# Kernel optimization log

Measured on AMD Instinct MI355X. Metric: run time of the kernel, lower is better.

## Reference

```python
import jax, jax.numpy as jnp
import numpy as np

N = 49152       # nodes
EH = 8192       # hyperedges (star nodes)
M = N + EH
F = 256         # num_features == expan_dim == MLP_hidden
D = 256
HEADS = 8
CHUNK = 1024
NE_N = 10 * N   # nnz of N x N sparse mats
NE_M = 10 * M   # nnz of M x M sparse mats


def spmm(row, col, val, X, n):
    # sparse [n, m] (COO) @ dense X [m, d] -> [n, d]
    return jax.ops.segment_sum(val[:, None] * X[col], row, num_segments=n)


def expan_net(x, row, col, val, Ws, bs, n):
    # 2-layer GCN: (A @ (X @ W) + b), ReLU between; dropout is identity in eval.
    h = spmm(row, col, val, x @ Ws[0], n) + bs[0]
    h = jax.nn.relu(h)
    return spmm(row, col, val, h @ Ws[1], n) + bs[1]


def chunked_mha(q, k, v, in_w, in_b, out_w, out_b):
    # torch nn.MultiheadAttention on unbatched [L, D] chunks of size CHUNK
    n, d = q.shape
    c = n // CHUNK
    dh = d // HEADS
    wq, wk, wv = jnp.split(in_w, 3, axis=0)
    bq, bk, bv = jnp.split(in_b, 3)
    def resh(t):
        return t.reshape(c, CHUNK, HEADS, dh)
    qh = resh(q @ wq.T + bq)
    kh = resh(k @ wk.T + bk)
    vh = resh(v @ wv.T + bv)
    scale = 1.0 / np.sqrt(dh)
    scores = jnp.einsum('clhe,cmhe->chlm', qh, kh) * scale  # [c,H,CHUNK,CHUNK]
    attn = jax.nn.softmax(scores, axis=-1)
    out = jnp.einsum('chlm,cmhe->clhe', attn, vh).reshape(n, d)
    return out @ out_w.T + out_b


def setup_inputs():
    key = jax.random.key(0)
    ks = iter(jax.random.split(key, 64))
    nrm = lambda shape, s=1.0: jax.random.normal(next(ks), shape, dtype=jnp.float32) * s
    uni = lambda shape: jax.random.uniform(next(ks), shape, dtype=jnp.float32)
    ridx = lambda shape, hi: jax.random.randint(next(ks), shape, 0, hi, dtype=jnp.int32)
    inp = {'x': nrm((N, F))}
    for nm, ne, hi in [('A_cg', NE_N, N), ('A_hyp', NE_N, N), ('A_sg', NE_M, M),
                       ('L_cg', NE_N, N), ('L_hyp', NE_N, N), ('L_sg', NE_M, M)]:
        inp[nm + '_row'] = ridx((ne,), hi)
        inp[nm + '_col'] = ridx((ne,), hi)
        inp[nm + '_val'] = uni((ne,)) * 0.1
    for p in ['cg', 'hg', 'sg']:
        inp[p + '_W'] = nrm((2, F, D), 0.05)
        inp[p + '_b'] = nrm((2, D), 0.05)
    for p in ['sn_hyp', 'sn_cg', 'sn_sg']:
        inp[p + '_W'] = nrm((D, D), 0.05)
        inp[p + '_b'] = nrm((D,), 0.05)
    for p in ['spa', 'spe']:
        for q in ['hyp', 'star', 'clq']:
            inp[f'{p}_{q}_W'] = nrm((D, D), 0.05)
            inp[f'{p}_{q}_b'] = nrm((D,), 0.05)
        inp[p + '_in_w'] = nrm((3 * D, D), 0.05)
        inp[p + '_in_b'] = nrm((3 * D,), 0.05)
        inp[p + '_out_w'] = nrm((D, D), 0.05)
        inp[p + '_out_b'] = nrm((D,), 0.05)
    return inp


def reference(x,
              A_cg_row, A_cg_col, A_cg_val, A_hyp_row, A_hyp_col, A_hyp_val,
              A_sg_row, A_sg_col, A_sg_val, L_cg_row, L_cg_col, L_cg_val,
              L_hyp_row, L_hyp_col, L_hyp_val, L_sg_row, L_sg_col, L_sg_val,
              cg_W, cg_b, hg_W, hg_b, sg_W, sg_b,
              sn_hyp_W, sn_hyp_b, sn_cg_W, sn_cg_b, sn_sg_W, sn_sg_b,
              spa_hyp_W, spa_hyp_b, spa_star_W, spa_star_b, spa_clq_W, spa_clq_b,
              spa_in_w, spa_in_b, spa_out_w, spa_out_b,
              spe_hyp_W, spe_hyp_b, spe_star_W, spe_star_b, spe_clq_W, spe_clq_b,
              spe_in_w, spe_in_b, spe_out_w, spe_out_b):
    n = x.shape[0]
    # star features: nodes first, zero-init hyperedge rows (v_mask == [True]*N+[False]*EH)
    x_star = jnp.concatenate([x, jnp.zeros((EH, x.shape[1]), x.dtype)], axis=0)
    # 1. Expansion graph convolutions
    cg_feat = expan_net(x, A_cg_row, A_cg_col, A_cg_val, cg_W, cg_b, n)
    hg_feat = expan_net(x, A_hyp_row, A_hyp_col, A_hyp_val, hg_W, hg_b, n)
    sg_feat = expan_net(x_star, A_sg_row, A_sg_col, A_sg_val, sg_W, sg_b, n + EH)
    X_star, S_star = sg_feat[:n], sg_feat[n:]
    # 2. SmoothNet: linear then Laplacian spmm
    X_hyp = spmm(L_hyp_row, L_hyp_col, L_hyp_val, hg_feat @ sn_hyp_W.T + sn_hyp_b, n)
    X_cg = spmm(L_cg_row, L_cg_col, L_cg_val, cg_feat @ sn_cg_W.T + sn_cg_b, n)
    X_sg = spmm(L_sg_row, L_sg_col, L_sg_val, sg_feat @ sn_sg_W.T + sn_sg_b, n + EH)
    # 3. TAA attention (chunked MHA, Q/K/V = hyp/star/clique projections)
    X_spectral = chunked_mha(X_hyp @ spe_hyp_W.T + spe_hyp_b,
                             X_cg @ spe_star_W.T + spe_star_b,
                             X_sg[:n] @ spe_clq_W.T + spe_clq_b,
                             spe_in_w, spe_in_b, spe_out_w, spe_out_b)
    X_spatial = chunked_mha(hg_feat @ spa_hyp_W.T + spa_hyp_b,
                            cg_feat @ spa_star_W.T + spa_star_b,
                            X_star @ spa_clq_W.T + spa_clq_b,
                            spa_in_w, spa_in_b, spa_out_w, spa_out_b)
    taa = jnp.concatenate([X_spatial, X_spectral], axis=1)
    return taa, X_star, S_star
```

## Files before the change

kernel.cpp:

```cpp
#include <hip/hip_runtime.h>

#define NN 49152
#define EHN 8192
#define MM (NN + EHN)
#define FD 256
#define DD 256
#define NHEADS 8
#define DHEAD 32
#define CHK 1024
#define NEN (10 * NN)
#define NEM (10 * MM)
#define ROWS_TOT (4 * NN + 2 * MM)
#define ETOT (4 * NEN + 2 * NEM)

typedef __bf16 bf16x8 __attribute__((ext_vector_type(8)));
typedef unsigned short u16x8 __attribute__((ext_vector_type(8)));
typedef float f32x4 __attribute__((ext_vector_type(4)));

static __device__ __forceinline__ unsigned short f2bf(float f) {
  unsigned int u = __float_as_uint(f);
  unsigned int r = (u + 0x7FFFu + ((u >> 16) & 1u)) >> 16;
  return (unsigned short)r;
}
static __device__ __forceinline__ float bf2f(unsigned short u) {
  return __uint_as_float((unsigned int)u << 16);
}
static __device__ __forceinline__ unsigned int cvtpk(float a, float b) {
  unsigned int r;
  asm("v_cvt_pk_bf16_f32 %0, %1, %2" : "=v"(r) : "v"(a), "v"(b));
  return r;
}

struct CastJobs {
  const float* src[8];
  unsigned short* dst[8];
  int trans[8];
};
__global__ __launch_bounds__(256) void cast_w8_kernel(CastJobs jobs)
{
  int job = blockIdx.x >> 8;
  int i = (blockIdx.x & 255) * 256 + threadIdx.x;
  int n = i >> 8, k = i & 255;
  const float* src = jobs.src[job];
  float f = jobs.trans[job] ? src[(size_t)k * 256 + n] : src[i];
  jobs.dst[job][i] = f2bf(f);
}

__global__ __launch_bounds__(256) void combine_w_kernel(
    const float* __restrict__ Bw, const float* __restrict__ Aw,
    const float* __restrict__ ab, const float* __restrict__ bb,
    unsigned short* __restrict__ Wc, float* __restrict__ bc, float fscale)
{
  int n = blockIdx.x, t = threadIdx.x;
  __shared__ float shB[256];
  __shared__ float red[256];
  shB[t] = Bw[n * 256 + t];
  __syncthreads();
  float acc = 0.0f;
  #pragma unroll 8
  for (int j = 0; j < 256; ++j) acc += shB[j] * Aw[j * 256 + t];
  Wc[n * 256 + t] = f2bf(acc * fscale);
  red[t] = shB[t] * ab[t];
  __syncthreads();
  for (int off = 128; off; off >>= 1) {
    if (t < off) red[t] += red[t + off];
    __syncthreads();
  }
  if (t == 0) bc[n] = (red[0] + bb[n]) * fscale;
}

__global__ __launch_bounds__(256) void mm256f_kernel(
    const float* __restrict__ A, const float* __restrict__ B,
    float* __restrict__ C)
{
  int n = blockIdx.x, t = threadIdx.x;
  __shared__ float sa[256];
  sa[t] = A[n * 256 + t];
  __syncthreads();
  float acc = 0.0f;
  #pragma unroll 8
  for (int j = 0; j < 256; ++j) acc += sa[j] * B[j * 256 + t];
  C[n * 256 + t] = acc;
}

__global__ __launch_bounds__(256) void mm256b_kernel(
    const float* __restrict__ A, const float* __restrict__ B,
    unsigned short* __restrict__ W, float fs)
{
  int n = blockIdx.x, t = threadIdx.x;
  __shared__ float sa[256];
  sa[t] = A[n * 256 + t];
  __syncthreads();
  float acc = 0.0f;
  #pragma unroll 8
  for (int j = 0; j < 256; ++j) acc += sa[j] * B[j * 256 + t];
  W[n * 256 + t] = f2bf(acc * fs);
}

__global__ __launch_bounds__(256) void mv256_kernel(
    const float* __restrict__ W, const float* __restrict__ v,
    const float* __restrict__ add, float* __restrict__ outv, float fs)
{
  int t = threadIdx.x;
  __shared__ float sv[256];
  sv[t] = v[t];
  __syncthreads();
  float acc = 0.0f;
  #pragma unroll 8
  for (int k = 0; k < 256; ++k) acc += W[t * 256 + k] * sv[k];
  if (add) acc += add[t];
  outv[t] = fs * acc;
}

struct Gemm3 {
  const void* A[3];
  const unsigned short* W[3];
  const float* c0[3];
  const float* rs[3];
  const float* cvec[3];
  unsigned short* out[3];
  int bs1, bs2, btot;
};
template<int ABF>
__global__ __launch_bounds__(256) void gemm3_kernel(Gemm3 g)
{
  const int b = blockIdx.x;
  const int j = (b >= g.bs2) ? 2 : (b >= g.bs1 ? 1 : 0);
  const int bm = (b - (j == 2 ? g.bs2 : j == 1 ? g.bs1 : 0)) * 64;
  const void* Ain = g.A[j];
  const unsigned short* Wt = g.W[j];

  __shared__ __align__(16) char sA[2][4096];
  __shared__ __align__(16) char sB[2][16384];
  const int tid = threadIdx.x, lane = tid & 63, wid = tid >> 6;
  const int l15 = lane & 15, l4 = lane >> 4;

  f32x4 acc[16] = {};
  const int ar = tid >> 2, akq = (tid & 3) * 8;
  const int bn = tid;

  float4 fa0, fa1;
  u16x8 ua;
  u16x8 rb0, rb1, rb2, rb3;
  auto stage_load = [&](int k0) {
    if (ABF) {
      ua = *(const u16x8*)((const unsigned short*)Ain +
                           (size_t)(bm + ar) * 256 + k0 + akq);
    } else {
      const float* ap = (const float*)Ain + (size_t)(bm + ar) * 256 + k0 + akq;
      fa0 = *(const float4*)ap;
      fa1 = *(const float4*)(ap + 4);
    }
    const unsigned short* bp = Wt + (size_t)bn * 256 + k0;
    rb0 = *(const u16x8*)bp;        rb1 = *(const u16x8*)(bp + 8);
    rb2 = *(const u16x8*)(bp + 16); rb3 = *(const u16x8*)(bp + 24);
  };
  auto stage_write = [&](int buf) {
    u16x8 va;
    if (ABF) {
      va = ua;
    } else {
      va[0] = f2bf(fa0.x); va[1] = f2bf(fa0.y); va[2] = f2bf(fa0.z); va[3] = f2bf(fa0.w);
      va[4] = f2bf(fa1.x); va[5] = f2bf(fa1.y); va[6] = f2bf(fa1.z); va[7] = f2bf(fa1.w);
    }
    int aa = ((ar << 6) + (akq << 1)) ^ ((ar & 7) << 4);
    *(u16x8*)(sA[buf] + aa) = va;
    int bb = (bn << 6) ^ ((bn & 7) << 4);
    *(u16x8*)(sB[buf] + bb) = rb0;
    *(u16x8*)(sB[buf] + (bb ^ 16)) = rb1;
    *(u16x8*)(sB[buf] + (bb ^ 32)) = rb2;
    *(u16x8*)(sB[buf] + (bb ^ 48)) = rb3;
  };

  stage_load(0);
  stage_write(0);
  __syncthreads();
  int cur = 0;
  for (int it = 0; it < 8; ++it) {
    if (it < 7) stage_load((it + 1) * 32);
    int ra = wid * 16 + l15;
    bf16x8 af = *(const bf16x8*)(sA[cur] + ((ra << 6) + (l4 << 4) ^ ((ra & 7) << 4)));
    #pragma unroll
    for (int n4 = 0; n4 < 16; ++n4) {
      int rn = n4 * 16 + l15;
      bf16x8 bf = *(const bf16x8*)(sB[cur] + ((rn << 6) + (l4 << 4) ^ ((rn & 7) << 4)));
      acc[n4] = __builtin_amdgcn_mfma_f32_16x16x32_bf16(af, bf, acc[n4], 0, 0, 0);
    }
    __syncthreads();
    if (it < 7) {
      stage_write(cur ^ 1);
      __syncthreads();
      cur ^= 1;
    }
  }
  const int row = bm + wid * 16 + l4 * 4;
  const float* rs = g.rs[j];
  const float* c0 = g.c0[j];
  const float* cvec = g.cvec[j];
  unsigned short* Cout = g.out[j];
  float rsv[4];
  if (rs) {
    #pragma unroll
    for (int jj = 0; jj < 4; ++jj) rsv[jj] = rs[row + jj];
  }
  #pragma unroll
  for (int n4 = 0; n4 < 16; ++n4) {
    int col = n4 * 16 + l15;
    float base = c0 ? c0[col] : 0.0f;
    float cv = rs ? cvec[col] : 0.0f;
    #pragma unroll
    for (int jj = 0; jj < 4; ++jj) {
      float v = acc[n4][jj] + base;
      if (rs) v += rsv[jj] * cv;
      Cout[(size_t)(row + jj) * 256 + col] = f2bf(v);
    }
  }
}

__global__ __launch_bounds__(256) void gemmout_kernel(
    const unsigned short* __restrict__ Ain, const unsigned short* __restrict__ Wt,
    const float* __restrict__ c0, float* __restrict__ Cout, int coff)
{
  __shared__ __align__(16) char sA[2][4096];
  __shared__ __align__(16) char sB[2][16384];
  const int tid = threadIdx.x, lane = tid & 63, wid = tid >> 6;
  const int l15 = lane & 15, l4 = lane >> 4;
  const int bm = blockIdx.x * 64;

  f32x4 acc[16] = {};
  const int ar = tid >> 2, akq = (tid & 3) * 8;
  const int bn = tid;
  u16x8 ua, rb0, rb1, rb2, rb3;
  auto stage_load = [&](int k0) {
    ua = *(const u16x8*)(Ain + (size_t)(bm + ar) * 256 + k0 + akq);
    const unsigned short* bp = Wt + (size_t)bn * 256 + k0;
    rb0 = *(const u16x8*)bp;        rb1 = *(const u16x8*)(bp + 8);
    rb2 = *(const u16x8*)(bp + 16); rb3 = *(const u16x8*)(bp + 24);
  };
  auto stage_write = [&](int buf) {
    int aa = ((ar << 6) + (akq << 1)) ^ ((ar & 7) << 4);
    *(u16x8*)(sA[buf] + aa) = ua;
    int bb = (bn << 6) ^ ((bn & 7) << 4);
    *(u16x8*)(sB[buf] + bb) = rb0;
    *(u16x8*)(sB[buf] + (bb ^ 16)) = rb1;
    *(u16x8*)(sB[buf] + (bb ^ 32)) = rb2;
    *(u16x8*)(sB[buf] + (bb ^ 48)) = rb3;
  };
  stage_load(0);
  stage_write(0);
  __syncthreads();
  int cur = 0;
  for (int it = 0; it < 8; ++it) {
    if (it < 7) stage_load((it + 1) * 32);
    int ra = wid * 16 + l15;
    bf16x8 af = *(const bf16x8*)(sA[cur] + ((ra << 6) + (l4 << 4) ^ ((ra & 7) << 4)));
    #pragma unroll
    for (int n4 = 0; n4 < 16; ++n4) {
      int rn = n4 * 16 + l15;
      bf16x8 bf = *(const bf16x8*)(sB[cur] + ((rn << 6) + (l4 << 4) ^ ((rn & 7) << 4)));
      acc[n4] = __builtin_amdgcn_mfma_f32_16x16x32_bf16(af, bf, acc[n4], 0, 0, 0);
    }
    __syncthreads();
    if (it < 7) {
      stage_write(cur ^ 1);
      __syncthreads();
      cur ^= 1;
    }
  }
  const int row = bm + wid * 16 + l4 * 4;
  #pragma unroll
  for (int n4 = 0; n4 < 16; ++n4) {
    int col = n4 * 16 + l15;
    float base = c0[col];
    #pragma unroll
    for (int jj = 0; jj < 4; ++jj)
      Cout[(size_t)(row + jj) * 512 + coff + col] = acc[n4][jj] + base;
  }
}

struct CooPtrs {
  const int* rw[6];
  const int* cl[6];
  const float* vl[6];
};
static __device__ __forceinline__ void coo_block_resolve(
    int b, int& g, int& eb, int& rb)
{
  if      (b < 1920) { g = 0; eb = 0;    rb = 0; }
  else if (b < 3840) { g = 1; eb = 1920; rb = NN; }
  else if (b < 6080) { g = 2; eb = 3840; rb = 2 * NN; }
  else if (b < 8000) { g = 3; eb = 6080; rb = 2 * NN + MM; }
  else if (b < 9920) { g = 4; eb = 8000; rb = 3 * NN + MM; }
  else               { g = 5; eb = 9920; rb = 4 * NN + MM; }
}

__global__ __launch_bounds__(256) void count_all_kernel(
    CooPtrs coo, int* __restrict__ cnt)
{
  int g, eb, rb;
  coo_block_resolve(blockIdx.x, g, eb, rb);
  int e = (blockIdx.x - eb) * 256 + threadIdx.x;
  atomicAdd(&cnt[rb + coo.rw[g][e]], 1);
}

__global__ __launch_bounds__(256) void scan1_kernel(
    const int* __restrict__ cnt, int* __restrict__ bsum, int n)
{
  __shared__ int sh[256];
  int i = blockIdx.x * 256 + threadIdx.x;
  sh[threadIdx.x] = (i < n) ? cnt[i] : 0;
  __syncthreads();
  for (int off = 128; off; off >>= 1) {
    if (threadIdx.x < off) sh[threadIdx.x] += sh[threadIdx.x + off];
    __syncthreads();
  }
  if (threadIdx.x == 0) bsum[blockIdx.x] = sh[0];
}

__global__ __launch_bounds__(256) void scan2_kernel(int* __restrict__ bsum, int nb)
{
  __shared__ int sh[256];
  int t = threadIdx.x;
  int carry = 0;
  for (int base = 0; base < nb; base += 256) {
    int i = base + t;
    int v = (i < nb) ? bsum[i] : 0;
    sh[t] = v;
    __syncthreads();
    for (int off = 1; off < 256; off <<= 1) {
      int add = (t >= off) ? sh[t - off] : 0;
      __syncthreads();
      sh[t] += add;
      __syncthreads();
    }
    int incl = sh[t];
    int tot = sh[255];
    if (i < nb) bsum[i] = carry + incl - v;
    carry += tot;
    __syncthreads();
  }
}

__global__ __launch_bounds__(256) void scan3_kernel(
    const int* __restrict__ cnt, const int* __restrict__ bsum,
    int* __restrict__ rowptr, int* __restrict__ cntz, int n)
{
  __shared__ int sh[256];
  int i = blockIdx.x * 256 + threadIdx.x;
  int v = (i < n) ? cnt[i] : 0;
  sh[threadIdx.x] = v;
  __syncthreads();
  for (int off = 1; off < 256; off <<= 1) {
    int add = (threadIdx.x >= off) ? sh[threadIdx.x - off] : 0;
    __syncthreads();
    sh[threadIdx.x] += add;
    __syncthreads();
  }
  int incl = sh[threadIdx.x];
  int base = bsum[blockIdx.x];
  if (i < n) { rowptr[i] = base + incl - v; cntz[i] = 0; }
  if (i == n - 1) rowptr[n] = base + incl;
}

__global__ __launch_bounds__(256) void fill_all_kernel(
    CooPtrs coo, const int* __restrict__ P, int* __restrict__ cur,
    int2* __restrict__ epack)
{
  int g, eb, rb;
  coo_block_resolve(blockIdx.x, g, eb, rb);
  int e = (blockIdx.x - eb) * 256 + threadIdx.x;
  int grow = rb + coo.rw[g][e];
  int pos = P[grow] + atomicAdd(&cur[grow], 1);
  epack[pos] = make_int2(coo.cl[g][e], __float_as_int(coo.vl[g][e]));
}

__global__ __launch_bounds__(256) void rowsum_all_kernel(
    const int* __restrict__ P, const int2* __restrict__ epack,
    float* __restrict__ rsAll)
{
  int j = blockIdx.x * 256 + threadIdx.x;
  int g = j / NN;
  int r = j - g * NN;
  int grow = (g == 0 ? 2 * NN + MM : g == 1 ? 3 * NN + MM : 4 * NN + MM) + r;
  float s = 0.0f;
  int end = P[grow + 1];
  for (int e = P[grow]; e < end; ++e) s += __int_as_float(epack[e].y);
  rsAll[j] = s;
}

struct Spmm3 {
  const int* rowptr[3];
  const unsigned short* X[3];
  unsigned short* Y[3];
  float* Y2[3];
  const float* bias[3];
  int src_rows[3];
  int bs1, bs2;
};
__global__ __launch_bounds__(256) void spmm3_kernel(
    Spmm3 s, const int2* __restrict__ ep, int relu)
{
  const int b = blockIdx.x;
  const int j = (b >= s.bs2) ? 2 : (b >= s.bs1 ? 1 : 0);
  const int rblk = b - (j == 2 ? s.bs2 : j == 1 ? s.bs1 : 0);
  const int wave = threadIdx.x >> 6, lane = threadIdx.x & 63;
  const int r = rblk * 4 + wave;
  const int f0 = lane * 4;
  const int src_rows = s.src_rows[j];
  const unsigned short* X = s.X[j];
  const int* rowptr = s.rowptr[j];
  int e = rowptr[r], end = rowptr[r + 1];
  float a0 = 0.0f, a1 = 0.0f, a2 = 0.0f, a3 = 0.0f;
  for (; e + 3 < end; e += 4) {
    int2 cv0 = ep[e], cv1 = ep[e + 1], cv2 = ep[e + 2], cv3 = ep[e + 3];
    ushort4 x0 = {0,0,0,0}, x1 = {0,0,0,0}, x2 = {0,0,0,0}, x3 = {0,0,0,0};
    if (cv0.x < src_rows) x0 = *(const ushort4*)(X + (size_t)cv0.x * DD + f0);
    if (cv1.x < src_rows) x1 = *(const ushort4*)(X + (size_t)cv1.x * DD + f0);
    if (cv2.x < src_rows) x2 = *(const ushort4*)(X + (size_t)cv2.x * DD + f0);
    if (cv3.x < src_rows) x3 = *(const ushort4*)(X + (size_t)cv3.x * DD + f0);
    float v0 = __int_as_float(cv0.y), v1 = __int_as_float(cv1.y);
    float v2 = __int_as_float(cv2.y), v3 = __int_as_float(cv3.y);
    if (cv0.x < src_rows) { a0 += v0*bf2f(x0.x); a1 += v0*bf2f(x0.y); a2 += v0*bf2f(x0.z); a3 += v0*bf2f(x0.w); }
    if (cv1.x < src_rows) { a0 += v1*bf2f(x1.x); a1 += v1*bf2f(x1.y); a2 += v1*bf2f(x1.z); a3 += v1*bf2f(x1.w); }
    if (cv2.x < src_rows) { a0 += v2*bf2f(x2.x); a1 += v2*bf2f(x2.y); a2 += v2*bf2f(x2.z); a3 += v2*bf2f(x2.w); }
    if (cv3.x < src_rows) { a0 += v3*bf2f(x3.x); a1 += v3*bf2f(x3.y); a2 += v3*bf2f(x3.z); a3 += v3*bf2f(x3.w); }
  }
  for (; e < end; ++e) {
    int2 cv = ep[e];
    if (cv.x < src_rows) {
      float v = __int_as_float(cv.y);
      ushort4 xx = *(const ushort4*)(X + (size_t)cv.x * DD + f0);
      a0 += v * bf2f(xx.x); a1 += v * bf2f(xx.y);
      a2 += v * bf2f(xx.z); a3 += v * bf2f(xx.w);
    }
  }
  const float* bias = s.bias[j];
  if (bias) {
    a0 += bias[f0]; a1 += bias[f0 + 1]; a2 += bias[f0 + 2]; a3 += bias[f0 + 3];
  }
  if (relu) {
    a0 = fmaxf(a0, 0.0f); a1 = fmaxf(a1, 0.0f);
    a2 = fmaxf(a2, 0.0f); a3 = fmaxf(a3, 0.0f);
  }
  uint2 yb = { cvtpk(a0, a1), cvtpk(a2, a3) };
  *(uint2*)(s.Y[j] + (size_t)r * DD + f0) = yb;
  if (s.Y2[j]) {
    float4 yf = {a0, a1, a2, a3};
    *(float4*)(s.Y2[j] + (size_t)r * DD + f0) = yf;
  }
}

__global__ __launch_bounds__(256) void attn_mfma_kernel(
    const unsigned short* __restrict__ Q, const unsigned short* __restrict__ K,
    const unsigned short* __restrict__ V, unsigned short* __restrict__ O)
{
  __shared__ __align__(16) char sKb[4096];
  __shared__ __align__(16) char sVb[4096];
  __shared__ __align__(16) char sPb[8192];
  const int wgid = (blockIdx.x & 7) * 768 + (blockIdx.x >> 3);
  const int qb = wgid & 15, h = (wgid >> 4) & 7, c = wgid >> 7;
  const int tid = threadIdx.x, lane = tid & 63, wid = tid >> 6;
  const int l15 = lane & 15, l4 = lane >> 4;
  char* sPw = sPb + wid * 2048;
  const size_t base = (size_t)c * (CHK * DD) + (size_t)h * DHEAD;
  const int q0 = qb * 64 + wid * 16;

  bf16x8 qf = *(const bf16x8*)(Q + base + (size_t)(q0 + l15) * DD + l4 * 8);

  const int key_s = tid >> 2, dq = (tid & 3) * 8;
  const unsigned short* Kp = K + base + (size_t)key_s * DD + dq;
  const unsigned short* Vp = V + base + (size_t)key_s * DD + dq;
  const int kaddr = ((key_s << 6) + (dq << 1)) ^ ((key_s & 7) << 4);

  f32x4 oacc[2] = {};
  float m = -1e30f, l = 0.0f;
  const f32x4 zero = {};

  for (int kt = 0; kt < CHK; kt += 64) {
    __syncthreads();
    u16x8 kv = *(const u16x8*)Kp;  Kp += 64 * DD;
    u16x8 vv = *(const u16x8*)Vp;  Vp += 64 * DD;
    *(u16x8*)(sKb + kaddr) = kv;
    #pragma unroll
    for (int i = 0; i < 8; ++i) {
      int d = dq + i;
      int bb = ((d << 7) + (key_s << 1))
             ^ ((d & 7) << 4) ^ (((d >> 3) & 3) << 5);
      *(unsigned short*)(sVb + bb) = vv[i];
    }
    __syncthreads();

    f32x4 s[4];
    #pragma unroll
    for (int s4 = 0; s4 < 4; ++s4) {
      int key = s4 * 16 + l15;
      int ba = ((key << 6) + (l4 << 4)) ^ ((key & 7) << 4);
      bf16x8 kf = *(const bf16x8*)(sKb + ba);
      s[s4] = __builtin_amdgcn_mfma_f32_16x16x32_bf16(kf, qf, zero, 0, 0, 0);
    }
    float tmax = -1e30f;
    #pragma unroll
    for (int s4 = 0; s4 < 4; ++s4)
      #pragma unroll
      for (int j = 0; j < 4; ++j) tmax = fmaxf(tmax, s[s4][j]);
    tmax = fmaxf(tmax, __shfl_xor(tmax, 16));
    tmax = fmaxf(tmax, __shfl_xor(tmax, 32));
    bool skip = __all(tmax - m <= 8.0f);
    float mnew = skip ? m : fmaxf(m, tmax);
    if (!skip) {
      float corr = __builtin_amdgcn_exp2f(m - mnew);
      l *= corr;
      oacc[0] *= corr;
      oacc[1] *= corr;
    }
    float psum = 0.0f;
    float p[4][4];
    #pragma unroll
    for (int s4 = 0; s4 < 4; ++s4)
      #pragma unroll
      for (int j = 0; j < 4; ++j) {
        p[s4][j] = __builtin_amdgcn_exp2f(s[s4][j] - mnew);
        psum += p[s4][j];
      }
    psum += __shfl_xor(psum, 16);
    psum += __shfl_xor(psum, 32);
    l += psum;
    m = mnew;
    #pragma unroll
    for (int s4 = 0; s4 < 4; ++s4) {
      uint2 pk = { cvtpk(p[s4][0], p[s4][1]), cvtpk(p[s4][2], p[s4][3]) };
      int bp = ((l15 << 7) + (s4 << 5) + (l4 << 3)) ^ ((l15 & 7) << 4);
      *(uint2*)(sPw + bp) = pk;
    }
    __syncthreads();

    #pragma unroll
    for (int dh = 0; dh < 2; ++dh)
      #pragma unroll
      for (int kh = 0; kh < 2; ++kh) {
        int d = dh * 16 + l15;
        int ba = ((d << 7) + ((kh * 32 + l4 * 8) << 1))
               ^ ((d & 7) << 4) ^ (((d >> 3) & 3) << 5);
        bf16x8 vf = *(const bf16x8*)(sVb + ba);
        int bp = ((l15 << 7) + (kh << 6) + (l4 << 4)) ^ ((l15 & 7) << 4);
        bf16x8 pf = *(const bf16x8*)(sPw + bp);
        oacc[dh] = __builtin_amdgcn_mfma_f32_16x16x32_bf16(vf, pf, oacc[dh], 0, 0, 0);
      }
  }

  float inv = 1.0f / l;
  unsigned short* orow = O + base + (size_t)(q0 + l15) * DD;
  #pragma unroll
  for (int dh = 0; dh < 2; ++dh) {
    uint2 o2 = { cvtpk(oacc[dh][0] * inv, oacc[dh][1] * inv),
                 cvtpk(oacc[dh][2] * inv, oacc[dh][3] * inv) };
    *(uint2*)(orow + dh * 16 + l4 * 4) = o2;
  }
}

__global__ __launch_bounds__(256) void fill_kernel(float* p, long n, float v)
{
  long i = (long)blockIdx.x * 256 + threadIdx.x;
  if (i < n) p[i] = v;
}

extern "C" void kernel_launch(void* const* d_in, const int* in_sizes, int n_in,
                              void* d_out, int out_size, void* d_ws, size_t ws_size,
                              hipStream_t stream)
{
  const float* x     = (const float*)d_in[0];
  const int*   Acg_r = (const int*)d_in[1];
  const int*   Acg_c = (const int*)d_in[2];
  const float* Acg_v = (const float*)d_in[3];
  const int*   Ahy_r = (const int*)d_in[4];
  const int*   Ahy_c = (const int*)d_in[5];
  const float* Ahy_v = (const float*)d_in[6];
  const int*   Asg_r = (const int*)d_in[7];
  const int*   Asg_c = (const int*)d_in[8];
  const float* Asg_v = (const float*)d_in[9];
  const int*   Lcg_r = (const int*)d_in[10];
  const int*   Lcg_c = (const int*)d_in[11];
  const float* Lcg_v = (const float*)d_in[12];
  const int*   Lhy_r = (const int*)d_in[13];
  const int*   Lhy_c = (const int*)d_in[14];
  const float* Lhy_v = (const float*)d_in[15];
  const int*   Lsg_r = (const int*)d_in[16];
  const int*   Lsg_c = (const int*)d_in[17];
  const float* Lsg_v = (const float*)d_in[18];
  const float* cg_W  = (const float*)d_in[19];
  const float* cg_b  = (const float*)d_in[20];
  const float* hg_W  = (const float*)d_in[21];
  const float* hg_b  = (const float*)d_in[22];
  const float* sg_W  = (const float*)d_in[23];
  const float* sg_b  = (const float*)d_in[24];
  const float* snh_W = (const float*)d_in[25];
  const float* snh_b = (const float*)d_in[26];
  const float* snc_W = (const float*)d_in[27];
  const float* snc_b = (const float*)d_in[28];
  const float* sns_W = (const float*)d_in[29];
  const float* sns_b = (const float*)d_in[30];
  const float* spa_hyp_W  = (const float*)d_in[31];
  const float* spa_hyp_b  = (const float*)d_in[32];
  const float* spa_star_W = (const float*)d_in[33];
  const float* spa_star_b = (const float*)d_in[34];
  const float* spa_clq_W  = (const float*)d_in[35];
  const float* spa_clq_b  = (const float*)d_in[36];
  const float* spa_in_w   = (const float*)d_in[37];
  const float* spa_in_b   = (const float*)d_in[38];
  const float* spa_out_w  = (const float*)d_in[39];
  const float* spa_out_b  = (const float*)d_in[40];
  const float* spe_hyp_W  = (const float*)d_in[41];
  const float* spe_hyp_b  = (const float*)d_in[42];
  const float* spe_star_W = (const float*)d_in[43];
  const float* spe_star_b = (const float*)d_in[44];
  const float* spe_clq_W  = (const float*)d_in[45];
  const float* spe_clq_b  = (const float*)d_in[46];
  const float* spe_in_w   = (const float*)d_in[47];
  const float* spe_in_b   = (const float*)d_in[48];
  const float* spe_out_w  = (const float*)d_in[49];
  const float* spe_out_b  = (const float*)d_in[50];

  float* out = (float*)d_out;

  const size_t NF = (size_t)NN * DD;
  const size_t MF = (size_t)MM * DD;
  const size_t WELEMS  = 14u * 65536u;
  const size_t need = (14 * NF + 3 * MF) * 2
                    + (size_t)ETOT * 8
                    + ((size_t)3 * NN + 65536 + 256 + 4096) * 4
                    + ((size_t)ROWS_TOT + 1 + ROWS_TOT + 2048) * 4
                    + WELEMS * 2;

  auto fill = [&](float v) {
    long tot = (long)out_size;
    fill_kernel<<<dim3((unsigned)((tot + 255) / 256)), 256, 0, stream>>>(out, tot, v);
  };
  if (ws_size < need)                        { fill(12.0f); return; }
  if (n_in != 51)                            { fill(16.0f); return; }
  if (in_sizes[0] != NN * FD)                { fill(20.0f); return; }
  if (in_sizes[3] != NEN)                    { fill(24.0f); return; }
  if (in_sizes[9] != NEM)                    { fill(28.0f); return; }
  if (in_sizes[19] != 2 * FD * DD)           { fill(32.0f); return; }
  if (in_sizes[37] != 3 * DD * DD)           { fill(36.0f); return; }
  if (out_size != NN * 512 + NN * DD + EHN * DD) { fill(40.0f); return; }

  unsigned short* Tcg = (unsigned short*)d_ws;
  unsigned short* Thy = Tcg + NF;
  unsigned short* Tsg = Thy + NF;
  unsigned short* Hcg = Tsg + NF;
  unsigned short* Hhy = Hcg + NF;
  unsigned short* Hsg = Hhy + NF;
  unsigned short* Usg = Hsg + MF;
  unsigned short* SG  = Usg + MF;
  unsigned short* CG  = SG + MF;
  unsigned short* HG  = CG + NF;
  unsigned short* LH  = HG + NF;
  unsigned short* LC  = LH + NF;
  unsigned short* LS  = LC + NF;
  unsigned short* QH  = LS + NF;
  unsigned short* KH  = QH + NF;
  unsigned short* VH  = KH + NF;
  unsigned short* AO  = VH + NF;
  unsigned short* Ucg = Tcg;
  unsigned short* Uhy = Thy;

  int2* epack = (int2*)(AO + NF);
  float* fp = (float*)(epack + ETOT);
  float* rsAll = fp;           fp += 3 * NN;
  float* tmp256 = fp;          fp += 65536;
  float* tmpv = fp;            fp += 256;
  float* CB = fp;              fp += 4096;
  int* P    = (int*)fp;
  int* cnt  = P + ROWS_TOT + 1;
  int* bsum = cnt + ROWS_TOT;
  unsigned short* WB = (unsigned short*)(bsum + 2048);

  int* rp_cg  = P;
  int* rp_hy  = P + NN;
  int* rp_sg  = P + 2 * NN;
  int* rp_Lcg = P + 2 * NN + MM;
  int* rp_Lhy = P + 3 * NN + MM;
  int* rp_Lsg = P + 4 * NN + MM;
  float* rs_c = rsAll;
  float* rs_h = rsAll + NN;
  float* rs_s = rsAll + 2 * NN;

  auto wslot = [&](int s) { return WB + (size_t)s * 65536; };
  auto cb    = [&](int s) { return CB + (size_t)s * 256; };

  auto combine = [&](const float* Bw, const float* Aw, const float* ab,
                     const float* bb, unsigned short* Wc, float* bcp, float fs) {
    combine_w_kernel<<<dim3(256), 256, 0, stream>>>(Bw, Aw, ab, bb, Wc, bcp, fs);
  };
  auto combine3 = [&](const float* w3, const float* b3, const float* pW,
                      const float* pb, const float* sW, const float* sb,
                      unsigned short* Wc, float* cvecp, float* c0p, float fs) {
    mm256f_kernel<<<dim3(256), 256, 0, stream>>>(pW, sW, tmp256);
    mm256b_kernel<<<dim3(256), 256, 0, stream>>>(w3, tmp256, Wc, fs);
    mv256_kernel<<<dim3(1), 256, 0, stream>>>(pW, sb, nullptr, tmpv, 1.0f);
    mv256_kernel<<<dim3(1), 256, 0, stream>>>(w3, tmpv, nullptr, cvecp, fs);
    mv256_kernel<<<dim3(1), 256, 0, stream>>>(w3, pb, b3, c0p, fs);
  };

  const float fsQ = 0.17677669529663687f * 1.4426950408889634f;

  {
    CastJobs jobs;
    jobs.src[0] = cg_W;           jobs.dst[0] = wslot(0);  jobs.trans[0] = 1;
    jobs.src[1] = cg_W + FD * DD; jobs.dst[1] = wslot(1);  jobs.trans[1] = 1;
    jobs.src[2] = hg_W;           jobs.dst[2] = wslot(2);  jobs.trans[2] = 1;
    jobs.src[3] = hg_W + FD * DD; jobs.dst[3] = wslot(3);  jobs.trans[3] = 1;
    jobs.src[4] = sg_W;           jobs.dst[4] = wslot(4);  jobs.trans[4] = 1;
    jobs.src[5] = sg_W + FD * DD; jobs.dst[5] = wslot(5);  jobs.trans[5] = 1;
    jobs.src[6] = spa_out_w;      jobs.dst[6] = wslot(12); jobs.trans[6] = 0;
    jobs.src[7] = spe_out_w;      jobs.dst[7] = wslot(13); jobs.trans[7] = 0;
    cast_w8_kernel<<<dim3(8 * 256), 256, 0, stream>>>(jobs);
  }
  combine(spa_in_w,                spa_hyp_W,  spa_hyp_b,  spa_in_b,          wslot(6), cb(0), fsQ);
  combine(spa_in_w + DD * DD,      spa_star_W, spa_star_b, spa_in_b + DD,     wslot(7), cb(1), 1.0f);
  combine(spa_in_w + 2 * DD * DD,  spa_clq_W,  spa_clq_b,  spa_in_b + 2 * DD, wslot(8), cb(2), 1.0f);
  combine3(spe_in_w,               spe_in_b,            spe_hyp_W,  spe_hyp_b,  snh_W, snh_b, wslot(9),  cb(3), cb(4), fsQ);
  combine3(spe_in_w + DD * DD,     spe_in_b + DD,       spe_star_W, spe_star_b, snc_W, snc_b, wslot(10), cb(5), cb(6), 1.0f);
  combine3(spe_in_w + 2 * DD * DD, spe_in_b + 2 * DD,   spe_clq_W,  spe_clq_b,  sns_W, sns_b, wslot(11), cb(7), cb(8), 1.0f);

  {
    CooPtrs coo;
    coo.rw[0] = Acg_r; coo.cl[0] = Acg_c; coo.vl[0] = Acg_v;
    coo.rw[1] = Ahy_r; coo.cl[1] = Ahy_c; coo.vl[1] = Ahy_v;
    coo.rw[2] = Asg_r; coo.cl[2] = Asg_c; coo.vl[2] = Asg_v;
    coo.rw[3] = Lcg_r; coo.cl[3] = Lcg_c; coo.vl[3] = Lcg_v;
    coo.rw[4] = Lhy_r; coo.cl[4] = Lhy_c; coo.vl[4] = Lhy_v;
    coo.rw[5] = Lsg_r; coo.cl[5] = Lsg_c; coo.vl[5] = Lsg_v;
    hipMemsetAsync(cnt, 0, (size_t)ROWS_TOT * 4, stream);
    count_all_kernel<<<dim3(ETOT / 256), 256, 0, stream>>>(coo, cnt);
    scan1_kernel<<<dim3(ROWS_TOT / 256), 256, 0, stream>>>(cnt, bsum, ROWS_TOT);
    scan2_kernel<<<dim3(1), 256, 0, stream>>>(bsum, ROWS_TOT / 256);
    scan3_kernel<<<dim3(ROWS_TOT / 256), 256, 0, stream>>>(cnt, bsum, P, cnt, ROWS_TOT);
    fill_all_kernel<<<dim3(ETOT / 256), 256, 0, stream>>>(coo, P, cnt, epack);
    rowsum_all_kernel<<<dim3(3 * NN / 256), 256, 0, stream>>>(P, epack, rsAll);
  }

  {
    Gemm3 g = {};
    for (int j = 0; j < 3; ++j) { g.A[j] = x; g.c0[j] = nullptr; g.rs[j] = nullptr; }
    g.W[0] = wslot(0); g.out[0] = Tcg;
    g.W[1] = wslot(2); g.out[1] = Thy;
    g.W[2] = wslot(4); g.out[2] = Tsg;
    g.bs1 = 768; g.bs2 = 1536; g.btot = 2304;
    gemm3_kernel<0><<<dim3(2304), 256, 0, stream>>>(g);
  }
  {
    Spmm3 s = {};
    s.rowptr[0] = rp_cg; s.X[0] = Tcg; s.Y[0] = Hcg; s.Y2[0] = nullptr; s.bias[0] = cg_b; s.src_rows[0] = NN;
    s.rowptr[1] = rp_hy; s.X[1] = Thy; s.Y[1] = Hhy; s.Y2[1] = nullptr; s.bias[1] = hg_b; s.src_rows[1] = NN;
    s.rowptr[2] = rp_sg; s.X[2] = Tsg; s.Y[2] = Hsg; s.Y2[2] = nullptr; s.bias[2] = sg_b; s.src_rows[2] = NN;
    s.bs1 = NN / 4; s.bs2 = 2 * (NN / 4);
    spmm3_kernel<<<dim3(2 * (NN / 4) + MM / 4), 256, 0, stream>>>(s, epack, 1);
  }
  {
    Gemm3 g = {};
    g.A[0] = Hcg; g.W[0] = wslot(1); g.out[0] = Ucg;
    g.A[1] = Hhy; g.W[1] = wslot(3); g.out[1] = Uhy;
    g.A[2] = Hsg; g.W[2] = wslot(5); g.out[2] = Usg;
    for (int j = 0; j < 3; ++j) { g.c0[j] = nullptr; g.rs[j] = nullptr; }
    g.bs1 = NN / 64; g.bs2 = 2 * (NN / 64); g.btot = 2 * (NN / 64) + MM / 64;
    gemm3_kernel<1><<<dim3(2 * (NN / 64) + MM / 64), 256, 0, stream>>>(g);
  }
  {
    Spmm3 s = {};
    s.rowptr[0] = rp_cg; s.X[0] = Ucg; s.Y[0] = CG; s.Y2[0] = nullptr; s.bias[0] = cg_b + DD; s.src_rows[0] = NN;
    s.rowptr[1] = rp_hy; s.X[1] = Uhy; s.Y[1] = HG; s.Y2[1] = nullptr; s.bias[1] = hg_b + DD; s.src_rows[1] = NN;
    s.rowptr[2] = rp_sg; s.X[2] = Usg; s.Y[2] = SG; s.Y2[2] = out + (size_t)NN * 512; s.bias[2] = sg_b + DD; s.src_rows[2] = MM;
    s.bs1 = NN / 4; s.bs2 = 2 * (NN / 4);
    spmm3_kernel<<<dim3(2 * (NN / 4) + MM / 4), 256, 0, stream>>>(s, epack, 0);
  }
  {
    Spmm3 s = {};
    s.rowptr[0] = rp_Lhy; s.X[0] = HG; s.Y[0] = LH; s.Y2[0] = nullptr; s.bias[0] = nullptr; s.src_rows[0] = NN;
    s.rowptr[1] = rp_Lcg; s.X[1] = CG; s.Y[1] = LC; s.Y2[1] = nullptr; s.bias[1] = nullptr; s.src_rows[1] = NN;
    s.rowptr[2] = rp_Lsg; s.X[2] = SG; s.Y[2] = LS; s.Y2[2] = nullptr; s.bias[2] = nullptr; s.src_rows[2] = MM;
    s.bs1 = NN / 4; s.bs2 = 2 * (NN / 4);
    spmm3_kernel<<<dim3(3 * (NN / 4)), 256, 0, stream>>>(s, epack, 0);
  }

  {
    Gemm3 g = {};
    g.A[0] = LH; g.W[0] = wslot(9);  g.c0[0] = cb(4); g.rs[0] = rs_h; g.cvec[0] = cb(3); g.out[0] = QH;
    g.A[1] = LC; g.W[1] = wslot(10); g.c0[1] = cb(6); g.rs[1] = rs_c; g.cvec[1] = cb(5); g.out[1] = KH;
    g.A[2] = LS; g.W[2] = wslot(11); g.c0[2] = cb(8); g.rs[2] = rs_s; g.cvec[2] = cb(7); g.out[2] = VH;
    g.bs1 = 768; g.bs2 = 1536; g.btot = 2304;
    gemm3_kernel<1><<<dim3(2304), 256, 0, stream>>>(g);
  }
  attn_mfma_kernel<<<dim3(6144), 256, 0, stream>>>(QH, KH, VH, AO);
  gemmout_kernel<<<dim3(NN / 64), 256, 0, stream>>>(AO, wslot(13), spe_out_b, out, 256);

  {
    Gemm3 g = {};
    g.A[0] = HG; g.W[0] = wslot(6); g.c0[0] = cb(0); g.rs[0] = nullptr; g.out[0] = QH;
    g.A[1] = CG; g.W[1] = wslot(7); g.c0[1] = cb(1); g.rs[1] = nullptr; g.out[1] = KH;
    g.A[2] = SG; g.W[2] = wslot(8); g.c0[2] = cb(2); g.rs[2] = nullptr; g.out[2] = VH;
    g.bs1 = 768; g.bs2 = 1536; g.btot = 2304;
    gemm3_kernel<1><<<dim3(2304), 256, 0, stream>>>(g);
  }
  attn_mfma_kernel<<<dim3(6144), 256, 0, stream>>>(QH, KH, VH, AO);
  gemmout_kernel<<<dim3(NN / 64), 256, 0, stream>>>(AO, wslot(12), spa_out_b, out, 0);
}
```

Baseline: 1.603 ms.

## Batch spectral and spatial attention and output GEMMs into single launches

The spectral and spatial branches are now processed by one attention launch and one output-projection launch each covering both jobs, instead of four separate launches. The spatial Q/K/V and attention outputs are placed in buffers that are dead by that point, so both branches can coexist. The goal is to fill the GPU better and remove launch and tail gaps. It also rewrites the softmax row-max as a three-operand max tree and changes the swizzle of the P tile in shared memory, which could alter LDS bank conflicts.

Measured after the change: 1.632 ms. About the same (+1.8%).

```diff
diff --git a/kernel.cpp b/kernel.cpp
--- a/kernel.cpp
+++ b/kernel.cpp
@@ -29,6 +29,9 @@
   unsigned int r;
   asm("v_cvt_pk_bf16_f32 %0, %1, %2" : "=v"(r) : "v"(a), "v"(b));
   return r;
+}
+static __device__ __forceinline__ float max3f(float a, float b, float c) {
+  return fmaxf(fmaxf(a, b), c);
 }
 
 struct CastJobs {
@@ -217,15 +220,24 @@
   }
 }
 
-__global__ __launch_bounds__(256) void gemmout_kernel(
-    const unsigned short* __restrict__ Ain, const unsigned short* __restrict__ Wt,
-    const float* __restrict__ c0, float* __restrict__ Cout, int coff)
-{
+__global__ __launch_bounds__(256) void gemmout2_kernel(
+    const unsigned short* __restrict__ A0, const unsigned short* __restrict__ W0,
+    const float* __restrict__ b0,
+    const unsigned short* __restrict__ A1, const unsigned short* __restrict__ W1,
+    const float* __restrict__ b1,
+    float* __restrict__ Cout)
+{
+  const int job = blockIdx.x >= (NN / 64);
+  const int bm = (blockIdx.x - (job ? NN / 64 : 0)) * 64;
+  const unsigned short* Ain = job ? A1 : A0;
+  const unsigned short* Wt  = job ? W1 : W0;
+  const float* c0 = job ? b1 : b0;
+  const int coff = job ? 0 : 256;
+
   __shared__ __align__(16) char sA[2][4096];
   __shared__ __align__(16) char sB[2][16384];
   const int tid = threadIdx.x, lane = tid & 63, wid = tid >> 6;
   const int l15 = lane & 15, l4 = lane >> 4;
-  const int bm = blockIdx.x * 64;
 
   f32x4 acc[16] = {};
   const int ar = tid >> 2, akq = (tid & 3) * 8;
@@ -450,15 +462,24 @@
   }
 }
 
-__global__ __launch_bounds__(256) void attn_mfma_kernel(
-    const unsigned short* __restrict__ Q, const unsigned short* __restrict__ K,
-    const unsigned short* __restrict__ V, unsigned short* __restrict__ O)
+__global__ __launch_bounds__(256) void attn2_kernel(
+    const unsigned short* __restrict__ Q1, const unsigned short* __restrict__ K1,
+    const unsigned short* __restrict__ V1, unsigned short* __restrict__ O1,
+    const unsigned short* __restrict__ Q2, const unsigned short* __restrict__ K2,
+    const unsigned short* __restrict__ V2, unsigned short* __restrict__ O2)
 {
   __shared__ __align__(16) char sKb[4096];
   __shared__ __align__(16) char sVb[4096];
   __shared__ __align__(16) char sPb[8192];
-  const int wgid = (blockIdx.x & 7) * 768 + (blockIdx.x >> 3);
-  const int qb = wgid & 15, h = (wgid >> 4) & 7, c = wgid >> 7;
+  const int wgid = (blockIdx.x & 7) * 1536 + (blockIdx.x >> 3);
+  const int qb = wgid & 15, h = (wgid >> 4) & 7, cc = wgid >> 7;
+  const int job = cc >= 48;
+  const int c = cc - (job ? 48 : 0);
+  const unsigned short* Q = job ? Q2 : Q1;
+  const unsigned short* K = job ? K2 : K1;
+  const unsigned short* V = job ? V2 : V1;
+  unsigned short* O = job ? O2 : O1;
+
   const int tid = threadIdx.x, lane = tid & 63, wid = tid >> 6;
   const int l15 = lane & 15, l4 = lane >> 4;
   char* sPw = sPb + wid * 2048;
@@ -498,11 +519,12 @@
       bf16x8 kf = *(const bf16x8*)(sKb + ba);
       s[s4] = __builtin_amdgcn_mfma_f32_16x16x32_bf16(kf, qf, zero, 0, 0, 0);
     }
-    float tmax = -1e30f;
-    #pragma unroll
-    for (int s4 = 0; s4 < 4; ++s4)
-      #pragma unroll
-      for (int j = 0; j < 4; ++j) tmax = fmaxf(tmax, s[s4][j]);
+    float t0 = max3f(s[0][0], s[0][1], s[0][2]);
+    float t1 = max3f(s[0][3], s[1][0], s[1][1]);
+    float t2 = max3f(s[1][2], s[1][3], s[2][0]);
+    float t3 = max3f(s[2][1], s[2][2], s[2][3]);
+    float t4 = max3f(s[3][0], s[3][1], s[3][2]);
+    float tmax = max3f(max3f(t0, t1, t2), fmaxf(t3, t4), s[3][3]);
     tmax = fmaxf(tmax, __shfl_xor(tmax, 16));
     tmax = fmaxf(tmax, __shfl_xor(tmax, 32));
     bool skip = __all(tmax - m <= 8.0f);
@@ -529,7 +551,7 @@
     #pragma unroll
     for (int s4 = 0; s4 < 4; ++s4) {
       uint2 pk = { cvtpk(p[s4][0], p[s4][1]), cvtpk(p[s4][2], p[s4][3]) };
-      int bp = ((l15 << 7) + (s4 << 5) + (l4 << 3)) ^ ((l15 & 7) << 4);
+      int bp = ((l15 << 7) + (s4 << 5) + (l4 << 3)) ^ ((l15 & 3) << 5);
       *(uint2*)(sPw + bp) = pk;
     }
     __syncthreads();
@@ -542,7 +564,7 @@
         int ba = ((d << 7) + ((kh * 32 + l4 * 8) << 1))
                ^ ((d & 7) << 4) ^ (((d >> 3) & 3) << 5);
         bf16x8 vf = *(const bf16x8*)(sVb + ba);
-        int bp = ((l15 << 7) + (kh << 6) + (l4 << 4)) ^ ((l15 & 7) << 4);
+        int bp = ((l15 << 7) + (kh << 6) + (l4 << 4)) ^ ((l15 & 3) << 5);
         bf16x8 pf = *(const bf16x8*)(sPw + bp);
         oacc[dh] = __builtin_amdgcn_mfma_f32_16x16x32_bf16(vf, pf, oacc[dh], 0, 0, 0);
       }
@@ -660,11 +682,17 @@
   unsigned short* QH  = LS + NF;
   unsigned short* KH  = QH + NF;
   unsigned short* VH  = KH + NF;
-  unsigned short* AO  = VH + NF;
+  unsigned short* AOx = VH + NF;
   unsigned short* Ucg = Tcg;
   unsigned short* Uhy = Thy;
-
-  int2* epack = (int2*)(AO + NF);
+  unsigned short* Q2  = LH;
+  unsigned short* K2  = LC;
+  unsigned short* V2  = LS;
+  unsigned short* AO1 = Hcg;
+  unsigned short* AO2 = Hhy;
+  (void)AOx;
+
+  int2* epack = (int2*)(AOx + NF);
   float* fp = (float*)(epack + ETOT);
   float* rsAll = fp;           fp += 3 * NN;
   float* tmp256 = fp;          fp += 65536;
@@ -791,17 +819,18 @@
     g.bs1 = 768; g.bs2 = 1536; g.btot = 2304;
     gemm3_kernel<1><<<dim3(2304), 256, 0, stream>>>(g);
   }
-  attn_mfma_kernel<<<dim3(6144), 256, 0, stream>>>(QH, KH, VH, AO);
-  gemmout_kernel<<<dim3(NN / 64), 256, 0, stream>>>(AO, wslot(13), spe_out_b, out, 256);
-
   {
     Gemm3 g = {};
-    g.A[0] = HG; g.W[0] = wslot(6); g.c0[0] = cb(0); g.rs[0] = nullptr; g.out[0] = QH;
-    g.A[1] = CG; g.W[1] = wslot(7); g.c0[1] = cb(1); g.rs[1] = nullptr; g.out[1] = KH;
-    g.A[2] = SG; g.W[2] = wslot(8); g.c0[2] = cb(2); g.rs[2] = nullptr; g.out[2] = VH;
+    g.A[0] = HG; g.W[0] = wslot(6); g.c0[0] = cb(0); g.rs[0] = nullptr; g.out[0] = Q2;
+    g.A[1] = CG; g.W[1] = wslot(7); g.c0[1] = cb(1); g.rs[1] = nullptr; g.out[1] = K2;
+    g.A[2] = SG; g.W[2] = wslot(8); g.c0[2] = cb(2); g.rs[2] = nullptr; g.out[2] = V2;
     g.bs1 = 768; g.bs2 = 1536; g.btot = 2304;
     gemm3_kernel<1><<<dim3(2304), 256, 0, stream>>>(g);
   }
-  attn_mfma_kernel<<<dim3(6144), 256, 0, stream>>>(QH, KH, VH, AO);
-  gemmout_kernel<<<dim3(NN / 64), 256, 0, stream>>>(AO, wslot(12), spa_out_b, out, 0);
-}
+  attn2_kernel<<<dim3(12288), 256, 0, stream>>>(QH, KH, VH, AO1,
+                                                Q2, K2, V2, AO2);
+  gemmout2_kernel<<<dim3(2 * (NN / 64)), 256, 0, stream>>>(
+      AO1, wslot(13), spe_out_b,
+      AO2, wslot(12), spa_out_b,
+      out);
+}
```
